# Kernel tuning notes

Measured on AMD Instinct MI355X. Metric: run time of the kernel, lower is better.

The kernel has to match this reference:

```python
import jax, jax.numpy as jnp
import numpy as np

D, H = 128, 8
N_NODE, N_SRC = 50000, 100000
E_NBR, E_INC = 800000, 200000


def _seg_softmax(scores, idx, n):
    # scores: [E, H]; segmented softmax over segments given by idx
    mx = jax.ops.segment_max(scores, idx, num_segments=n)
    ex = jnp.exp(scores - mx[idx])
    sm = jax.ops.segment_sum(ex, idx, num_segments=n)
    return ex / (sm[idx] + 1e-12)


def _ln(x, g, b):
    m = jnp.mean(x, -1, keepdims=True)
    v = jnp.mean((x - m) ** 2, -1, keepdims=True)
    return g * (x - m) / jnp.sqrt(v + 1e-5) + b


def setup_inputs() -> dict:
    key = jax.random.key(0)
    ks = jax.random.split(key, 24)
    s = 1.0 / np.sqrt(D)
    inp = {
        'X': jax.random.normal(ks[0], (N_NODE, D), jnp.float32),
        'X_src': jax.random.normal(ks[1], (N_SRC, D), jnp.float32),
        'W_qkv': jax.random.normal(ks[2], (D, 3 * D), jnp.float32) * s,
        'w_bias': jax.random.normal(ks[3], (D, H), jnp.float32) * s,
        'W_gate': jax.random.normal(ks[4], (D, D), jnp.float32) * s,
        'b_gate': jnp.zeros((D,), jnp.float32),
        'W_o': jax.random.normal(ks[5], (D, D), jnp.float32) * s,
        'W_q': jax.random.normal(ks[6], (D, D), jnp.float32) * s,
        'W_kv': jax.random.normal(ks[7], (D, 2 * D), jnp.float32) * s,
        'w_bias_tgt': jax.random.normal(ks[8], (D, H), jnp.float32) * s,
        'w_bias_src': jax.random.normal(ks[9], (D, H), jnp.float32) * s,
        'W_gate_tgt': jax.random.normal(ks[10], (D, D), jnp.float32) * s,
        'b_gate_tgt': jnp.zeros((D,), jnp.float32),
        'W_gate_src': jax.random.normal(ks[11], (D, D), jnp.float32) * s,
        'b_gate_src': jnp.zeros((D,), jnp.float32),
        'W_o2': jax.random.normal(ks[12], (D, D), jnp.float32) * s,
        'ln1_g': jnp.ones((D,), jnp.float32),
        'ln1_b': jnp.zeros((D,), jnp.float32),
        'ln2_g': jnp.ones((D,), jnp.float32),
        'ln2_b': jnp.zeros((D,), jnp.float32),
        'nbr_src': jax.random.randint(ks[13], (E_NBR,), 0, N_NODE),
        'nbr_dst': jax.random.randint(ks[14], (E_NBR,), 0, N_NODE),
        'inc_tgt': jax.random.randint(ks[15], (E_INC,), 0, N_NODE),
        'inc_src': jax.random.randint(ks[16], (E_INC,), 0, N_SRC),
    }
    return inp


def reference(X, X_src, W_qkv, w_bias, W_gate, b_gate, W_o, W_q, W_kv,
              w_bias_tgt, w_bias_src, W_gate_tgt, b_gate_tgt, W_gate_src,
              b_gate_src, W_o2, ln1_g, ln1_b, ln2_g, ln2_b,
              nbr_src, nbr_dst, inc_tgt, inc_src):
    N = X.shape[0]
    dk = D // H
    scale = 1.0 / np.sqrt(dk)

    # --- SparseNeighbourhoodSelfAttn on level-0 cells ---
    qkv = (X @ W_qkv).reshape(N, 3, H, dk)
    Q, K, V = qkv[:, 0], qkv[:, 1], qkv[:, 2]            # [N,H,dk]
    scores = jnp.sum(Q[nbr_src] * K[nbr_dst], -1) * scale + (X @ w_bias)[nbr_src]  # [E,H]
    attn = _seg_softmax(scores, nbr_src, N)
    out = jax.ops.segment_sum(attn[..., None] * V[nbr_dst], nbr_src, num_segments=N)  # [N,H,dk]
    gate = jax.nn.sigmoid(X @ W_gate + b_gate).reshape(N, H, dk)
    sa = (gate * out).reshape(N, D) @ W_o
    h = _ln(X + sa, ln1_g, ln1_b)

    # --- SparseTopologicalCrossAttn from level-1 cells ---
    Qc = (h @ W_q).reshape(N, H, dk)
    kv = (X_src @ W_kv).reshape(-1, 2, H, dk)
    Kc, Vc = kv[:, 0], kv[:, 1]
    sc = (jnp.sum(Qc[inc_tgt] * Kc[inc_src], -1) * scale
          + (h @ w_bias_tgt)[inc_tgt] + (X_src @ w_bias_src)[inc_src])  # [Ei,H]
    attn_c = _seg_softmax(sc, inc_tgt, N)
    g_src = jax.nn.sigmoid(X_src @ W_gate_src + b_gate_src).reshape(-1, H, dk)
    out_c = jax.ops.segment_sum(attn_c[..., None] * (g_src[inc_src] * Vc[inc_src]),
                                inc_tgt, num_segments=N)
    g_tgt = jax.nn.sigmoid(h @ W_gate_tgt + b_gate_tgt).reshape(N, H, dk)
    ca = (g_tgt * out_c).reshape(N, D) @ W_o2
    return _ln(h + ca, ln2_g, ln2_b)
```

## Files before the change

### kernel.cpp

```cpp
#include <hip/hip_runtime.h>
#include <stdint.h>

__device__ __forceinline__ float bf_lo(uint32_t w) { return __uint_as_float(w << 16); }
__device__ __forceinline__ float bf_hi(uint32_t w) { return __uint_as_float(w & 0xffff0000u); }
__device__ __forceinline__ float bfu(uint16_t u) { return __uint_as_float((uint32_t)u << 16); }
__device__ __forceinline__ uint16_t f2bf(float f) {
    uint32_t u = __float_as_uint(f);
    uint32_t r = ((u >> 16) & 1u) + 0x7fffu;
    return (uint16_t)((u + r) >> 16);
}
__device__ __forceinline__ uint32_t pk2bf(float a, float b) {
    return (uint32_t)f2bf(a) | ((uint32_t)f2bf(b) << 16);
}
__device__ __forceinline__ void gload_lds16(const void* g, void* l) {
    __builtin_amdgcn_global_load_lds(
        (const __attribute__((address_space(1))) void*)g,
        (__attribute__((address_space(3))) void*)l, 16, 0, 0);
}

typedef __attribute__((ext_vector_type(8))) short bf16x8;
typedef __attribute__((ext_vector_type(4))) float f32x4;

#define LOG2E 1.4426950408889634f
#define QSC2  (0.25f * LOG2E)

#define M_BF16 0
#define M_QS   1
#define M_SIG  2
#define M_KVIK 3
#define M_KVIV 4
#define M_GV   5
#define M_LN1  6
#define M_LN2  7
#define M_B8   8

struct GemmJob {
    const uint16_t* A; const uint16_t* WT; const float* bias;
    const uint16_t* aux; const void* resid;
    const float* lng; const float* lnb;
    void* out; int M; int mode;
};
struct GemmJobs { GemmJob j[6]; };

__global__ __launch_bounds__(256) void multi_gemm_k(GemmJobs jobs)
{
    __shared__ uint16_t As[128 * 128];
    __shared__ uint16_t Ws[128 * 128];
    const GemmJob jb = jobs.j[blockIdx.y];
    const int m0 = blockIdx.x * 128;
    if (m0 >= jb.M) return;
    const int tid = threadIdx.x;
    const int wid = tid >> 6;
    const int lane = tid & 63;

    {
        const uint16_t* Ab = jb.A + (size_t)m0 * 128;
        const uint16_t* Wb = jb.WT;
#pragma unroll
        for (int it = 0; it < 8; ++it) {
            int idx = it * 256 + tid;
            int r = idx >> 4, c = idx & 15;
            int gc = c ^ (r & 7);
            uint16_t* ldsA = As + (size_t)(it * 256 + wid * 64) * 8;
            uint16_t* ldsW = Ws + (size_t)(it * 256 + wid * 64) * 8;
            gload_lds16(Ab + (size_t)r * 128 + gc * 8, ldsA);
            gload_lds16(Wb + (size_t)r * 128 + gc * 8, ldsW);
        }
    }
    __syncthreads();

    const int wr = wid >> 1, wc = wid & 1;
    const int l15 = lane & 15, l4 = lane >> 4;
    const int mode = jb.mode;

    if (mode == M_B8) {
        f32x4 acc[4];
#pragma unroll
        for (int i = 0; i < 4; i++) acc[i] = (f32x4){0.f, 0.f, 0.f, 0.f};
#pragma unroll
        for (int kk = 0; kk < 4; ++kk) {
            bf16x8 af0;
            {
                int r = l15;
                int cc = (kk * 4 + l4) ^ (r & 7);
                af0 = *(const bf16x8*)(Ws + r * 128 + cc * 8);
            }
#pragma unroll
            for (int mi = 0; mi < 4; ++mi) {
                int r = wr * 64 + mi * 16 + l15;
                int cc = (kk * 4 + l4) ^ (r & 7);
                bf16x8 bf = *(const bf16x8*)(As + r * 128 + cc * 8);
                acc[mi] = __builtin_amdgcn_mfma_f32_16x16x32_bf16(af0, bf, acc[mi], 0, 0, 0);
            }
        }
        if (wc == 0 && l4 < 2) {
#pragma unroll
            for (int mi = 0; mi < 4; ++mi) {
                int gm = m0 + wr * 64 + mi * 16 + l15;
                if (gm < jb.M) {
                    f32x4 v = acc[mi];
                    *(float4*)((float*)jb.out + (size_t)gm * 8 + l4 * 4) =
                        make_float4(v.x, v.y, v.z, v.w);
                }
            }
        }
        return;
    }

    f32x4 acc[4][4];
#pragma unroll
    for (int i = 0; i < 4; i++)
#pragma unroll
        for (int j = 0; j < 4; j++) acc[i][j] = (f32x4){0.f, 0.f, 0.f, 0.f};

#pragma unroll
    for (int kk = 0; kk < 4; ++kk) {
        bf16x8 af[4], bff[4];
#pragma unroll
        for (int ni = 0; ni < 4; ++ni) {
            int r = wc * 64 + ni * 16 + l15;
            int cc = (kk * 4 + l4) ^ (r & 7);
            af[ni] = *(const bf16x8*)(Ws + r * 128 + cc * 8);
        }
#pragma unroll
        for (int mi = 0; mi < 4; ++mi) {
            int r = wr * 64 + mi * 16 + l15;
            int cc = (kk * 4 + l4) ^ (r & 7);
            bff[mi] = *(const bf16x8*)(As + r * 128 + cc * 8);
        }
#pragma unroll
        for (int ni = 0; ni < 4; ++ni)
#pragma unroll
            for (int mi = 0; mi < 4; ++mi)
                acc[ni][mi] = __builtin_amdgcn_mfma_f32_16x16x32_bf16(
                    af[ni], bff[mi], acc[ni][mi], 0, 0, 0);
    }

    if (mode == M_LN1 || mode == M_LN2) {
        __syncthreads();
        float* redS = (float*)Ws;
        float* redQ = redS + 256;
        float ps[4], qs[4];
#pragma unroll
        for (int mi = 0; mi < 4; ++mi) {
            int row = wr * 64 + mi * 16 + l15;
            int gm = m0 + row;
            float sum = 0.f, sq = 0.f;
#pragma unroll
            for (int ni = 0; ni < 4; ++ni) {
                int gn = wc * 64 + ni * 16 + l4 * 4;
                float r0 = 0.f, r1 = 0.f, r2 = 0.f, r3 = 0.f;
                if (gm < jb.M) {
                    if (mode == M_LN1) {
                        float4 rv = *(const float4*)((const float*)jb.resid + (size_t)gm * 128 + gn);
                        r0 = rv.x; r1 = rv.y; r2 = rv.z; r3 = rv.w;
                    } else {
                        ushort4 rv = *(const ushort4*)((const uint16_t*)jb.resid + (size_t)gm * 128 + gn);
                        r0 = bfu(rv.x); r1 = bfu(rv.y); r2 = bfu(rv.z); r3 = bfu(rv.w);
                    }
                }
                f32x4 t = acc[ni][mi];
                t.x += r0; t.y += r1; t.z += r2; t.w += r3;
                acc[ni][mi] = t;
                sum += t.x + t.y + t.z + t.w;
                sq  += t.x * t.x + t.y * t.y + t.z * t.z + t.w * t.w;
            }
            sum += __shfl_xor(sum, 16); sum += __shfl_xor(sum, 32);
            sq  += __shfl_xor(sq, 16);  sq  += __shfl_xor(sq, 32);
            ps[mi] = sum; qs[mi] = sq;
        }
        if (l4 == 0) {
#pragma unroll
            for (int mi = 0; mi < 4; ++mi) {
                int row = wr * 64 + mi * 16 + l15;
                redS[row * 2 + wc] = ps[mi];
                redQ[row * 2 + wc] = qs[mi];
            }
        }
        __syncthreads();
#pragma unroll
        for (int mi = 0; mi < 4; ++mi) {
            int row = wr * 64 + mi * 16 + l15;
            int gm = m0 + row;
            if (gm >= jb.M) continue;
            float S = redS[row * 2] + redS[row * 2 + 1];
            float Q = redQ[row * 2] + redQ[row * 2 + 1];
            float mean = S * (1.f / 128.f);
            float var  = Q * (1.f / 128.f) - mean * mean;
            float rstd = rsqrtf(var + 1e-5f);
#pragma unroll
            for (int ni = 0; ni < 4; ++ni) {
                int gn = wc * 64 + ni * 16 + l4 * 4;
                float4 gg = *(const float4*)(jb.lng + gn);
                float4 bb = *(const float4*)(jb.lnb + gn);
                f32x4 t = acc[ni][mi];
                float o0 = gg.x * (t.x - mean) * rstd + bb.x;
                float o1 = gg.y * (t.y - mean) * rstd + bb.y;
                float o2 = gg.z * (t.z - mean) * rstd + bb.z;
                float o3 = gg.w * (t.w - mean) * rstd + bb.w;
                if (mode == M_LN1) {
                    ushort4 o;
                    o.x = f2bf(o0); o.y = f2bf(o1); o.z = f2bf(o2); o.w = f2bf(o3);
                    *(ushort4*)((uint16_t*)jb.out + (size_t)gm * 128 + gn) = o;
                } else {
                    *(float4*)((float*)jb.out + (size_t)gm * 128 + gn) =
                        make_float4(o0, o1, o2, o3);
                }
            }
        }
        return;
    }

#pragma unroll
    for (int mi = 0; mi < 4; ++mi) {
        int gm = m0 + wr * 64 + mi * 16 + l15;
        if (gm >= jb.M) continue;
#pragma unroll
        for (int ni = 0; ni < 4; ++ni) {
            int gn = wc * 64 + ni * 16 + l4 * 4;
            f32x4 v = acc[ni][mi];
            if (mode == M_SIG || mode == M_GV) {
                float4 bb = *(const float4*)(jb.bias + gn);
                v.x = 1.f / (1.f + __expf(-(v.x + bb.x)));
                v.y = 1.f / (1.f + __expf(-(v.y + bb.y)));
                v.z = 1.f / (1.f + __expf(-(v.z + bb.z)));
                v.w = 1.f / (1.f + __expf(-(v.w + bb.w)));
            }
            if (mode == M_QS) { v.x *= QSC2; v.y *= QSC2; v.z *= QSC2; v.w *= QSC2; }
            if (mode == M_GV) {
                ushort4 vs = *(const ushort4*)(jb.aux + (size_t)gm * 128 + gn);
                v.x *= bfu(vs.x); v.y *= bfu(vs.y); v.z *= bfu(vs.z); v.w *= bfu(vs.w);
            }
            if (mode == M_KVIK || mode == M_KVIV || mode == M_GV) {
                int which = (mode == M_KVIK) ? 0 : 2;
                uint16_t* op = (uint16_t*)jb.out + (size_t)gm * 256 + gn * 2 + which;
                *reinterpret_cast<uint32_t*>(op)     = pk2bf(v.x, v.y);
                *reinterpret_cast<uint32_t*>(op + 4) = pk2bf(v.z, v.w);
            } else {
                ushort4 o;
                o.x = f2bf(v.x); o.y = f2bf(v.y); o.z = f2bf(v.z); o.w = f2bf(v.w);
                *reinterpret_cast<ushort4*>((uint16_t*)jb.out + (size_t)gm * 128 + gn) = o;
            }
        }
    }
}

__global__ void castbf2_k(const float* __restrict__ in1, uint16_t* __restrict__ out1, int n1,
                          const float* __restrict__ in2, uint16_t* __restrict__ out2, int n2,
                          int* __restrict__ zero256)
{
    if (blockIdx.x == 0 && threadIdx.x < 256) zero256[threadIdx.x] = 0;
    int i = blockIdx.x * blockDim.x + threadIdx.x;
    int stride = gridDim.x * blockDim.x;
    for (; i < n1 + n2; i += stride) {
        float4 v;
        ushort4 o;
        if (i < n1) v = reinterpret_cast<const float4*>(in1)[i];
        else        v = reinterpret_cast<const float4*>(in2)[i - n1];
        o.x = f2bf(v.x); o.y = f2bf(v.y); o.z = f2bf(v.z); o.w = f2bf(v.w);
        if (i < n1) reinterpret_cast<ushort4*>(out1)[i] = o;
        else        reinterpret_cast<ushort4*>(out2)[i - n1] = o;
    }
}

struct WT14 { const float* src[14]; uint16_t* dst[14]; int nc[14]; int coff[14]; };
__global__ void castWT14_k(WT14 jb)
{
    int y = blockIdx.y;
    const float* W = jb.src[y];
    uint16_t* WT = jb.dst[y];
    int nc = jb.nc[y], coff = jb.coff[y];
    int i = blockIdx.x * 256 + threadIdx.x;
    int k = i >> 7, n = i & 127;
    float v;
    if (nc == 8) v = (n < 8) ? W[k * 8 + n] * LOG2E : 0.f;
    else         v = W[(size_t)k * nc + coff + n];
    WT[(size_t)n * 128 + k] = f2bf(v);
}

#define NBKT_MAX 256

__global__ __launch_bounds__(256) void binH_k(
    const int* __restrict__ s1, const int* __restrict__ s2,
    int* __restrict__ bktcnt, int E1, int E2, int N, int shift, int nbkt, int chunk)
{
    __shared__ int hist[NBKT_MAX];
    int t = threadIdx.x;
    for (int i = t; i < nbkt; i += 256) hist[i] = 0;
    __syncthreads();
    int Et = E1 + E2;
    int base = blockIdx.x * chunk;
    int end = min(base + chunk, Et);
    for (int i = base + t; i < end; i += 256) {
        int seg = (i < E1) ? s1[i] : N + s2[i - E1];
        atomicAdd(&hist[seg >> shift], 1);
    }
    __syncthreads();
    for (int i = t; i < nbkt; i += 256)
        if (hist[i]) atomicAdd(&bktcnt[i], hist[i]);
}

__global__ __launch_bounds__(256) void bktscan_k(
    const int* __restrict__ bktcnt, int* __restrict__ bktbase,
    int* __restrict__ bktcur, int nbkt)
{
    __shared__ int wt[4];
    int t = threadIdx.x, lane = t & 63, w = t >> 6;
    int v = (t < nbkt) ? bktcnt[t] : 0;
    int s = v;
#pragma unroll
    for (int o = 1; o < 64; o <<= 1) { int x = __shfl_up(s, o); if (lane >= o) s += x; }
    if (lane == 63) wt[w] = s;
    __syncthreads();
    int add = 0;
    for (int i = 0; i < w; i++) add += wt[i];
    int excl = add + s - v;
    if (t < nbkt) { bktbase[t] = excl; bktcur[t] = excl; }
    if (t == nbkt - 1) bktbase[nbkt] = excl + v;
}

__global__ __launch_bounds__(256) void binA_k(
    const int* __restrict__ s1, const int* __restrict__ p1,
    const int* __restrict__ s2, const int* __restrict__ p2,
    int* __restrict__ bktcur, uint2* __restrict__ tmp,
    int E1, int E2, int N, int shift, int nbkt, int chunk)
{
    __shared__ int hist[NBKT_MAX];
    __shared__ int lcur[NBKT_MAX];
    int t = threadIdx.x;
    int Et = E1 + E2;
    int base = blockIdx.x * chunk;
    int end = min(base + chunk, Et);
    for (int i = t; i < nbkt; i += 256) hist[i] = 0;
    __syncthreads();
    for (int i = base + t; i < end; i += 256) {
        int seg = (i < E1) ? s1[i] : N + s2[i - E1];
        atomicAdd(&hist[seg >> shift], 1);
    }
    __syncthreads();
    for (int i = t; i < nbkt; i += 256) {
        int c = hist[i];
        lcur[i] = c ? atomicAdd(&bktcur[i], c) : 0;
    }
    __syncthreads();
    for (int i = base + t; i < end; i += 256) {
        int seg, pay;
        if (i < E1) { seg = s1[i]; pay = p1[i]; }
        else        { seg = N + s2[i - E1]; pay = p2[i - E1]; }
        int p = atomicAdd(&lcur[seg >> shift], 1);
        tmp[p] = make_uint2((uint32_t)seg, (uint32_t)pay);
    }
}

__global__ __launch_bounds__(256) void binD_k(
    const uint2* __restrict__ tmp, const int* __restrict__ bktbase,
    int* __restrict__ offs, int* __restrict__ sorted, int NN, int spb, int Et)
{
    extern __shared__ int sh[];
    __shared__ int wt[4];
    int b = blockIdx.x, t = threadIdx.x;
    int s0 = b * spb;
    int segs = min(spb, NN - s0);
    for (int i = t; i < segs; i += 256) sh[i] = 0;
    __syncthreads();
    int p0 = bktbase[b], p1 = bktbase[b + 1];
    for (int i = p0 + t; i < p1; i += 256)
        atomicAdd(&sh[(int)tmp[i].x - s0], 1);
    __syncthreads();
    int e_per = spb >> 8;
    int loc[4]; int ls = 0;
#pragma unroll 4
    for (int j = 0; j < 4; ++j) {
        if (j < e_per) {
            int idx = t * e_per + j;
            int v = (idx < segs) ? sh[idx] : 0;
            loc[j] = ls; ls += v;
        }
    }
    int lane = t & 63, w = t >> 6;
    int sc = ls;
#pragma unroll
    for (int o = 1; o < 64; o <<= 1) { int x = __shfl_up(sc, o); if (lane >= o) sc += x; }
    if (lane == 63) wt[w] = sc;
    __syncthreads();
    int add = 0;
    for (int i = 0; i < w; i++) add += wt[i];
    int texcl = add + sc - ls;
#pragma unroll 4
    for (int j = 0; j < 4; ++j) {
        if (j < e_per) {
            int idx = t * e_per + j;
            if (idx < segs) {
                int pos = p0 + texcl + loc[j];
                offs[s0 + idx] = pos;
                sh[idx] = pos;
            }
        }
    }
    __syncthreads();
    for (int i = p0 + t; i < p1; i += 256) {
        uint2 pr = tmp[i];
        int p = atomicAdd(&sh[(int)pr.x - s0], 1);
        sorted[p] = (int)pr.y;
    }
    if (b == 0 && t == 0) offs[NN] = Et;
}

#define SEDGE(J, IDX)                                                            \
    {                                                                            \
        int dst = sdst[IDX];                                                     \
        uint2 kv = *reinterpret_cast<const uint2*>(kb + ((size_t)dst << 8));     \
        float s = q0 * bf_lo(kv.x) + q1 * bf_hi(kv.x);                           \
        s += __shfl_xor(s, 1); s += __shfl_xor(s, 2); s += __shfl_xor(s, 4);     \
        float w = exp2f(s + bs);                                                 \
        pa##J = fmaf(w, bf_lo(kv.y), pa##J);                                     \
        pb##J = fmaf(w, bf_hi(kv.y), pb##J);                                     \
        dn##J += w;                                                              \
    }

__global__ __launch_bounds__(256) void self_attn_k(
    const uint16_t* __restrict__ Qb, const uint16_t* __restrict__ kvi,
    const float* __restrict__ bias1,
    const int* __restrict__ offs, const int* __restrict__ sdst,
    const uint16_t* __restrict__ g16, uint16_t* __restrict__ Aout, int N)
{
    int lane = threadIdx.x & 63;
    int n = blockIdx.x * 4 + (threadIdx.x >> 6);
    if (n >= N) return;
    uint32_t qw = *reinterpret_cast<const uint32_t*>(Qb + (size_t)n * 128 + 2 * lane);
    float q0 = bf_lo(qw), q1 = bf_hi(qw);
    float bs = bias1[(size_t)n * 8 + (lane >> 3)];
    int e0 = offs[n], e1 = offs[n + 1];
    const uint16_t* kb = kvi + lane * 4;
    float dn0 = 0.f, pa0 = 0.f, pb0 = 0.f;
    float dn1 = 0.f, pa1 = 0.f, pb1 = 0.f;
    int e = e0;
    for (; e + 4 <= e1; e += 4) {
        SEDGE(0, e)
        SEDGE(1, e + 1)
        SEDGE(0, e + 2)
        SEDGE(1, e + 3)
    }
    for (; e < e1; ++e) SEDGE(0, e)
    float den = dn0 + dn1, a0 = pa0 + pa1, a1 = pb0 + pb1;
    float inv = 1.f / (den + 1e-30f);
    uint32_t gw = *reinterpret_cast<const uint32_t*>(g16 + (size_t)n * 128 + 2 * lane);
    a0 *= inv * bf_lo(gw); a1 *= inv * bf_hi(gw);
    *reinterpret_cast<uint32_t*>(Aout + (size_t)n * 128 + 2 * lane) = pk2bf(a0, a1);
}

#define CEDGE(J, IDX)                                                            \
    {                                                                            \
        int src = ssrc[IDX];                                                     \
        uint2 kv = *reinterpret_cast<const uint2*>(kb + ((size_t)src << 8));     \
        float bss = bias_s[(size_t)src * 8 + (lane >> 3)];                       \
        float s = q0 * bf_lo(kv.x) + q1 * bf_hi(kv.x);                           \
        s += __shfl_xor(s, 1); s += __shfl_xor(s, 2); s += __shfl_xor(s, 4);     \
        float w = exp2f(s + bt + bss);                                           \
        pa##J = fmaf(w, bf_lo(kv.y), pa##J);                                     \
        pb##J = fmaf(w, bf_hi(kv.y), pb##J);                                     \
        dn##J += w;                                                              \
    }

__global__ __launch_bounds__(256) void cross_attn_k(
    const uint16_t* __restrict__ Qcb, const float* __restrict__ bias_t,
    const uint16_t* __restrict__ kvgi, const float* __restrict__ bias_s,
    const int* __restrict__ offs, const int* __restrict__ ssrc,
    const uint16_t* __restrict__ g16, uint16_t* __restrict__ Aout, int N)
{
    int lane = threadIdx.x & 63;
    int n = blockIdx.x * 4 + (threadIdx.x >> 6);
    if (n >= N) return;
    uint32_t qw = *reinterpret_cast<const uint32_t*>(Qcb + (size_t)n * 128 + 2 * lane);
    float q0 = bf_lo(qw), q1 = bf_hi(qw);
    float bt = bias_t[(size_t)n * 8 + (lane >> 3)];
    int e0 = offs[n], e1 = offs[n + 1];
    const uint16_t* kb = kvgi + lane * 4;
    float dn0 = 0.f, pa0 = 0.f, pb0 = 0.f;
    float dn1 = 0.f, pa1 = 0.f, pb1 = 0.f;
    int e = e0;
    for (; e + 4 <= e1; e += 4) {
        CEDGE(0, e)
        CEDGE(1, e + 1)
        CEDGE(0, e + 2)
        CEDGE(1, e + 3)
    }
    for (; e < e1; ++e) CEDGE(0, e)
    float den = dn0 + dn1, a0 = pa0 + pa1, a1 = pb0 + pb1;
    float inv = 1.f / (den + 1e-30f);
    uint32_t gw = *reinterpret_cast<const uint32_t*>(g16 + (size_t)n * 128 + 2 * lane);
    a0 *= inv * bf_lo(gw); a1 *= inv * bf_hi(gw);
    *reinterpret_cast<uint32_t*>(Aout + (size_t)n * 128 + 2 * lane) = pk2bf(a0, a1);
}

static inline size_t smax_(size_t a, size_t b) { return a > b ? a : b; }

extern "C" void kernel_launch(void* const* d_in, const int* in_sizes, int n_in,
                              void* d_out, int out_size, void* d_ws, size_t ws_size,
                              hipStream_t stream)
{
    const float* X          = (const float*)d_in[0];
    const float* Xs         = (const float*)d_in[1];
    const float* W_qkv      = (const float*)d_in[2];
    const float* w_bias     = (const float*)d_in[3];
    const float* W_gate     = (const float*)d_in[4];
    const float* b_gate     = (const float*)d_in[5];
    const float* W_o        = (const float*)d_in[6];
    const float* W_q        = (const float*)d_in[7];
    const float* W_kv       = (const float*)d_in[8];
    const float* w_bias_tgt = (const float*)d_in[9];
    const float* w_bias_src = (const float*)d_in[10];
    const float* W_gate_tgt = (const float*)d_in[11];
    const float* b_gate_tgt = (const float*)d_in[12];
    const float* W_gate_src = (const float*)d_in[13];
    const float* b_gate_src = (const float*)d_in[14];
    const float* W_o2       = (const float*)d_in[15];
    const float* ln1_g      = (const float*)d_in[16];
    const float* ln1_b      = (const float*)d_in[17];
    const float* ln2_g      = (const float*)d_in[18];
    const float* ln2_b      = (const float*)d_in[19];
    const int* nbr_src      = (const int*)d_in[20];
    const int* nbr_dst      = (const int*)d_in[21];
    const int* inc_tgt      = (const int*)d_in[22];
    const int* inc_src      = (const int*)d_in[23];

    const int N  = in_sizes[0] / 128;
    const int NS = in_sizes[1] / 128;
    const int E1 = in_sizes[20];
    const int E2 = in_sizes[22];
    const int Et = E1 + E2;
    const int NN = 2 * N;
    const int Npad  = (N + 127) & ~127;
    const int NSpad = (NS + 127) & ~127;

    int shift = 9;
    while (((NN + (1 << shift) - 1) >> shift) > NBKT_MAX) ++shift;
    const int spb  = 1 << shift;
    const int nbkt = (NN + spb - 1) >> shift;

    char* ws = (char*)d_ws;
    size_t off = 0;
    auto alloc = [&](size_t bytes) -> void* {
        void* p = ws + off;
        off = (off + bytes + 255) & ~(size_t)255;
        return p;
    };

    uint16_t* Xb   = (uint16_t*)alloc((size_t)Npad * 128 * 2);
    uint16_t* Xsb  = (uint16_t*)alloc((size_t)NSpad * 128 * 2);
    uint16_t* WTq  = (uint16_t*)alloc((size_t)384 * 128 * 2);
    uint16_t* WTkv = (uint16_t*)alloc((size_t)256 * 128 * 2);
    uint16_t* WTg  = (uint16_t*)alloc((size_t)128 * 128 * 2);
    uint16_t* WTo  = (uint16_t*)alloc((size_t)128 * 128 * 2);
    uint16_t* WTq2 = (uint16_t*)alloc((size_t)128 * 128 * 2);
    uint16_t* WTgt = (uint16_t*)alloc((size_t)128 * 128 * 2);
    uint16_t* WTgs = (uint16_t*)alloc((size_t)128 * 128 * 2);
    uint16_t* WTo2 = (uint16_t*)alloc((size_t)128 * 128 * 2);
    uint16_t* WTb1 = (uint16_t*)alloc((size_t)128 * 128 * 2);
    uint16_t* WTbt = (uint16_t*)alloc((size_t)128 * 128 * 2);
    uint16_t* WTbs = (uint16_t*)alloc((size_t)128 * 128 * 2);
    size_t s1a = (size_t)Npad * 384 * 2;
    size_t s1b = (size_t)NSpad * 384 * 2;
    size_t s1c = (size_t)Et * 8;
    uint16_t* S1 = (uint16_t*)alloc(smax_(smax_(s1a, s1b), s1c));
    uint16_t* Qb   = S1;
    uint16_t* kvi  = S1 + (size_t)Npad * 128;
    uint16_t* kvgi = S1;
    uint16_t* V16  = S1 + (size_t)NSpad * 256;
    uint2*    tmp  = (uint2*)S1;
    uint16_t* g16  = (uint16_t*)alloc((size_t)N * 128 * 2);
    uint16_t* Qcb  = (uint16_t*)alloc((size_t)N * 128 * 2);
    uint16_t* Awo  = (uint16_t*)alloc((size_t)Npad * 128 * 2);
    uint16_t* hb   = (uint16_t*)alloc((size_t)Npad * 128 * 2);
    float*    b8a  = (float*)alloc((size_t)N * 8 * 4);
    float*    b8s  = (float*)alloc((size_t)NS * 8 * 4);
    int* offs   = (int*)alloc((size_t)(NN + 1) * 4);
    int* sorted = (int*)alloc((size_t)Et * 4);
    int* bktcnt = (int*)alloc((size_t)NBKT_MAX * 4);
    int* bktbase= (int*)alloc((size_t)(NBKT_MAX + 1) * 4);
    int* bktcur = (int*)alloc((size_t)NBKT_MAX * 4);
    (void)ws_size; (void)n_in; (void)out_size;

    const int gA  = Npad / 128;
    const int gAs = NSpad / 128;
    const int gW  = (N + 3) / 4;
    const int BINB = 128;
    const int chunk = (Et + BINB - 1) / BINB;

    castbf2_k<<<2048, 256, 0, stream>>>(X, Xb, N * 32, Xs, Xsb, NS * 32, bktcnt);
    {
        WT14 jb;
        jb.src[0] = W_qkv; jb.dst[0] = WTq;          jb.nc[0] = 384; jb.coff[0] = 0;
        jb.src[1] = W_qkv; jb.dst[1] = WTq + 16384;  jb.nc[1] = 384; jb.coff[1] = 128;
        jb.src[2] = W_qkv; jb.dst[2] = WTq + 32768;  jb.nc[2] = 384; jb.coff[2] = 256;
        jb.src[3] = W_kv;  jb.dst[3] = WTkv;         jb.nc[3] = 256; jb.coff[3] = 0;
        jb.src[4] = W_kv;  jb.dst[4] = WTkv + 16384; jb.nc[4] = 256; jb.coff[4] = 128;
        jb.src[5] = W_gate;     jb.dst[5] = WTg;  jb.nc[5] = 128; jb.coff[5] = 0;
        jb.src[6] = W_o;        jb.dst[6] = WTo;  jb.nc[6] = 128; jb.coff[6] = 0;
        jb.src[7] = W_q;        jb.dst[7] = WTq2; jb.nc[7] = 128; jb.coff[7] = 0;
        jb.src[8] = W_gate_tgt; jb.dst[8] = WTgt; jb.nc[8] = 128; jb.coff[8] = 0;
        jb.src[9] = W_gate_src; jb.dst[9] = WTgs; jb.nc[9] = 128; jb.coff[9] = 0;
        jb.src[10]= W_o2;       jb.dst[10]= WTo2; jb.nc[10]= 128; jb.coff[10]= 0;
        jb.src[11]= w_bias;     jb.dst[11]= WTb1; jb.nc[11]= 8;   jb.coff[11]= 0;
        jb.src[12]= w_bias_tgt; jb.dst[12]= WTbt; jb.nc[12]= 8;   jb.coff[12]= 0;
        jb.src[13]= w_bias_src; jb.dst[13]= WTbs; jb.nc[13]= 8;   jb.coff[13]= 0;
        castWT14_k<<<dim3(64, 14), 256, 0, stream>>>(jb);
    }

    binH_k<<<BINB, 256, 0, stream>>>(nbr_src, inc_tgt, bktcnt, E1, E2, N, shift, nbkt, chunk);
    bktscan_k<<<1, 256, 0, stream>>>(bktcnt, bktbase, bktcur, nbkt);
    binA_k<<<BINB, 256, 0, stream>>>(nbr_src, nbr_dst, inc_tgt, inc_src,
                                     bktcur, tmp, E1, E2, N, shift, nbkt, chunk);
    binD_k<<<nbkt, 256, spb * 4, stream>>>(tmp, bktbase, offs, sorted, NN, spb, Et);

    {
        GemmJobs jb{};
        jb.j[0] = { Xb, WTq,         nullptr, nullptr, nullptr, nullptr, nullptr, Qb,  N, M_QS };
        jb.j[1] = { Xb, WTq + 16384, nullptr, nullptr, nullptr, nullptr, nullptr, kvi, N, M_KVIK };
        jb.j[2] = { Xb, WTq + 32768, nullptr, nullptr, nullptr, nullptr, nullptr, kvi, N, M_KVIV };
        jb.j[3] = { Xb, WTg,         b_gate,  nullptr, nullptr, nullptr, nullptr, g16, N, M_SIG };
        jb.j[4] = { Xb, WTb1,        nullptr, nullptr, nullptr, nullptr, nullptr, b8a, N, M_B8 };
        multi_gemm_k<<<dim3(gA, 5), 256, 0, stream>>>(jb);
    }
    self_attn_k<<<gW, 256, 0, stream>>>(Qb, kvi, b8a, offs, sorted, g16, Awo, N);
    {
        GemmJobs jb{};
        jb.j[0] = { Awo, WTo, nullptr, nullptr, X, ln1_g, ln1_b, hb, N, M_LN1 };
        multi_gemm_k<<<dim3(gA, 1), 256, 0, stream>>>(jb);
    }
    {
        GemmJobs jb{};
        jb.j[0] = { hb,  WTq2,         nullptr,    nullptr, nullptr, nullptr, nullptr, Qcb,  N,  M_QS };
        jb.j[1] = { hb,  WTgt,         b_gate_tgt, nullptr, nullptr, nullptr, nullptr, g16,  N,  M_SIG };
        jb.j[2] = { Xsb, WTkv,         nullptr,    nullptr, nullptr, nullptr, nullptr, kvgi, NS, M_KVIK };
        jb.j[3] = { Xsb, WTkv + 16384, nullptr,    nullptr, nullptr, nullptr, nullptr, V16,  NS, M_BF16 };
        jb.j[4] = { hb,  WTbt,         nullptr,    nullptr, nullptr, nullptr, nullptr, b8a,  N,  M_B8 };
        multi_gemm_k<<<dim3(gAs, 5), 256, 0, stream>>>(jb);
    }
    {
        GemmJobs jb{};
        jb.j[0] = { Xsb, WTgs, b_gate_src, V16, nullptr, nullptr, nullptr, kvgi, NS, M_GV };
        jb.j[1] = { Xsb, WTbs, nullptr, nullptr, nullptr, nullptr, nullptr, b8s,  NS, M_B8 };
        multi_gemm_k<<<dim3(gAs, 2), 256, 0, stream>>>(jb);
    }
    cross_attn_k<<<gW, 256, 0, stream>>>(Qcb, b8a, kvgi, b8s, offs + N, sorted, g16, Awo, N);
    {
        GemmJobs jb{};
        jb.j[0] = { Awo, WTo2, nullptr, nullptr, hb, ln2_g, ln2_b, d_out, N, M_LN2 };
        multi_gemm_k<<<dim3(gA, 1), 256, 0, stream>>>(jb);
    }
}
```

Before: 339.5 us.

## Reuse A tile across jobs per block and drop histogram pass in edge binning

The GEMM kernel now stages the A tile once per block and loops over several weight matrices, replacing grid-y job dispatch that reloaded A for each job. The cross-attention source GEMMs are reordered so the V tile written by one job is consumed by the gated job inside the same block. Edge binning drops the histogram and scan kernels by using fixed-capacity buckets and writing per-segment end offsets. This cuts launches and A-tile traffic but lowers grid parallelism per launch and serializes jobs within a block; fixed bucket capacity could overflow on skewed inputs.

```diff
diff --git a/kernel.cpp b/kernel.cpp
--- a/kernel.cpp
+++ b/kernel.cpp
@@ -34,222 +34,234 @@
 #define M_LN2  7
 #define M_B8   8
 
-struct GemmJob {
-    const uint16_t* A; const uint16_t* WT; const float* bias;
-    const uint16_t* aux; const void* resid;
-    const float* lng; const float* lnb;
-    void* out; int M; int mode;
+struct GJob {
+    const uint16_t* WT; const float* bias; const uint16_t* aux;
+    const void* resid; const float* lng; const float* lnb;
+    void* out; int mode;
 };
-struct GemmJobs { GemmJob j[6]; };
-
-__global__ __launch_bounds__(256) void multi_gemm_k(GemmJobs jobs)
+struct GArgs { const uint16_t* A; int M; int njobs; GJob j[5]; };
+
+__device__ __forceinline__ void stage_tile(const uint16_t* __restrict__ g,
+                                           uint16_t* lds, int tid, int wid)
+{
+#pragma unroll
+    for (int it = 0; it < 8; ++it) {
+        int idx = it * 256 + tid;
+        int r = idx >> 4, c = idx & 15;
+        int gc = c ^ (r & 7);
+        gload_lds16(g + (size_t)r * 128 + gc * 8,
+                    lds + (size_t)(it * 256 + wid * 64) * 8);
+    }
+}
+
+__global__ __launch_bounds__(256) void gemmA_k(GArgs ga)
 {
     __shared__ uint16_t As[128 * 128];
     __shared__ uint16_t Ws[128 * 128];
-    const GemmJob jb = jobs.j[blockIdx.y];
-    const int m0 = blockIdx.x * 128;
-    if (m0 >= jb.M) return;
     const int tid = threadIdx.x;
     const int wid = tid >> 6;
     const int lane = tid & 63;
-
-    {
-        const uint16_t* Ab = jb.A + (size_t)m0 * 128;
-        const uint16_t* Wb = jb.WT;
-#pragma unroll
-        for (int it = 0; it < 8; ++it) {
-            int idx = it * 256 + tid;
-            int r = idx >> 4, c = idx & 15;
-            int gc = c ^ (r & 7);
-            uint16_t* ldsA = As + (size_t)(it * 256 + wid * 64) * 8;
-            uint16_t* ldsW = Ws + (size_t)(it * 256 + wid * 64) * 8;
-            gload_lds16(Ab + (size_t)r * 128 + gc * 8, ldsA);
-            gload_lds16(Wb + (size_t)r * 128 + gc * 8, ldsW);
-        }
-    }
+    const int m0 = blockIdx.x * 128;
+    const int M = ga.M;
+
+    stage_tile(ga.A + (size_t)m0 * 128, As, tid, wid);
+    stage_tile(ga.j[0].WT, Ws, tid, wid);
     __syncthreads();
 
     const int wr = wid >> 1, wc = wid & 1;
     const int l15 = lane & 15, l4 = lane >> 4;
-    const int mode = jb.mode;
-
-    if (mode == M_B8) {
-        f32x4 acc[4];
-#pragma unroll
-        for (int i = 0; i < 4; i++) acc[i] = (f32x4){0.f, 0.f, 0.f, 0.f};
-#pragma unroll
-        for (int kk = 0; kk < 4; ++kk) {
-            bf16x8 af0;
-            {
-                int r = l15;
-                int cc = (kk * 4 + l4) ^ (r & 7);
-                af0 = *(const bf16x8*)(Ws + r * 128 + cc * 8);
+
+    for (int jj = 0; ; ) {
+        const GJob jb = ga.j[jj];
+        const int mode = jb.mode;
+
+        if (mode == M_B8) {
+            f32x4 acc[4];
+#pragma unroll
+            for (int i = 0; i < 4; i++) acc[i] = (f32x4){0.f, 0.f, 0.f, 0.f};
+#pragma unroll
+            for (int kk = 0; kk < 4; ++kk) {
+                bf16x8 af0;
+                {
+                    int r = l15;
+                    int cc = (kk * 4 + l4) ^ (r & 7);
+                    af0 = *(const bf16x8*)(Ws + r * 128 + cc * 8);
+                }
+#pragma unroll
+                for (int mi = 0; mi < 4; ++mi) {
+                    int r = wr * 64 + mi * 16 + l15;
+                    int cc = (kk * 4 + l4) ^ (r & 7);
+                    bf16x8 bf = *(const bf16x8*)(As + r * 128 + cc * 8);
+                    acc[mi] = __builtin_amdgcn_mfma_f32_16x16x32_bf16(af0, bf, acc[mi], 0, 0, 0);
+                }
             }
-#pragma unroll
-            for (int mi = 0; mi < 4; ++mi) {
-                int r = wr * 64 + mi * 16 + l15;
-                int cc = (kk * 4 + l4) ^ (r & 7);
-                bf16x8 bf = *(const bf16x8*)(As + r * 128 + cc * 8);
-                acc[mi] = __builtin_amdgcn_mfma_f32_16x16x32_bf16(af0, bf, acc[mi], 0, 0, 0);
+            if (wc == 0 && l4 < 2) {
+#pragma unroll
+                for (int mi = 0; mi < 4; ++mi) {
+                    int gm = m0 + wr * 64 + mi * 16 + l15;
+                    if (gm < M) {
+                        f32x4 v = acc[mi];
+                        *(float4*)((float*)jb.out + (size_t)gm * 8 + l4 * 4) =
+                            make_float4(v.x, v.y, v.z, v.w);
+                    }
+                }
+            }
+        } else {
+            f32x4 acc[4][4];
+#pragma unroll
+            for (int i = 0; i < 4; i++)
+#pragma unroll
+                for (int j = 0; j < 4; j++) acc[i][j] = (f32x4){0.f, 0.f, 0.f, 0.f};
+
+#pragma unroll
+            for (int kk = 0; kk < 4; ++kk) {
+                bf16x8 af[4], bff[4];
+#pragma unroll
+                for (int ni = 0; ni < 4; ++ni) {
+                    int r = wc * 64 + ni * 16 + l15;
+                    int cc = (kk * 4 + l4) ^ (r & 7);
+                    af[ni] = *(const bf16x8*)(Ws + r * 128 + cc * 8);
+                }
+#pragma unroll
+                for (int mi = 0; mi < 4; ++mi) {
+                    int r = wr * 64 + mi * 16 + l15;
+                    int cc = (kk * 4 + l4) ^ (r & 7);
+                    bff[mi] = *(const bf16x8*)(As + r * 128 + cc * 8);
+                }
+#pragma unroll
+                for (int ni = 0; ni < 4; ++ni)
+#pragma unroll
+                    for (int mi = 0; mi < 4; ++mi)
+                        acc[ni][mi] = __builtin_amdgcn_mfma_f32_16x16x32_bf16(
+                            af[ni], bff[mi], acc[ni][mi], 0, 0, 0);
+            }
+
+            if (mode == M_LN1 || mode == M_LN2) {
+                __syncthreads();
+                float* redS = (float*)Ws;
+                float* redQ = redS + 256;
+                float ps[4], qs[4];
+#pragma unroll
+                for (int mi = 0; mi < 4; ++mi) {
+                    int row = wr * 64 + mi * 16 + l15;
+                    int gm = m0 + row;
+                    float sum = 0.f, sq = 0.f;
+#pragma unroll
+                    for (int ni = 0; ni < 4; ++ni) {
+                        int gn = wc * 64 + ni * 16 + l4 * 4;
+                        float r0 = 0.f, r1 = 0.f, r2 = 0.f, r3 = 0.f;
+                        if (gm < M) {
+                            if (mode == M_LN1) {
+                                float4 rv = *(const float4*)((const float*)jb.resid + (size_t)gm * 128 + gn);
+                                r0 = rv.x; r1 = rv.y; r2 = rv.z; r3 = rv.w;
+                            } else {
+                                ushort4 rv = *(const ushort4*)((const uint16_t*)jb.resid + (size_t)gm * 128 + gn);
+                                r0 = bfu(rv.x); r1 = bfu(rv.y); r2 = bfu(rv.z); r3 = bfu(rv.w);
+                            }
+                        }
+                        f32x4 t = acc[ni][mi];
+                        t.x += r0; t.y += r1; t.z += r2; t.w += r3;
+                        acc[ni][mi] = t;
+                        sum += t.x + t.y + t.z + t.w;
+                        sq  += t.x * t.x + t.y * t.y + t.z * t.z + t.w * t.w;
+                    }
+                    sum += __shfl_xor(sum, 16); sum += __shfl_xor(sum, 32);
+                    sq  += __shfl_xor(sq, 16);  sq  += __shfl_xor(sq, 32);
+                    ps[mi] = sum; qs[mi] = sq;
+                }
+                if (l4 == 0) {
+#pragma unroll
+                    for (int mi = 0; mi < 4; ++mi) {
+                        int row = wr * 64 + mi * 16 + l15;
+                        redS[row * 2 + wc] = ps[mi];
+                        redQ[row * 2 + wc] = qs[mi];
+                    }
+                }
+                __syncthreads();
+#pragma unroll
+                for (int mi = 0; mi < 4; ++mi) {
+                    int row = wr * 64 + mi * 16 + l15;
+                    int gm = m0 + row;
+                    if (gm >= M) continue;
+                    float S = redS[row * 2] + redS[row * 2 + 1];
+                    float Q = redQ[row * 2] + redQ[row * 2 + 1];
+                    float mean = S * (1.f / 128.f);
+                    float var  = Q * (1.f / 128.f) - mean * mean;
+                    float rstd = rsqrtf(var + 1e-5f);
+#pragma unroll
+                    for (int ni = 0; ni < 4; ++ni) {
+                        int gn = wc * 64 + ni * 16 + l4 * 4;
+                        float4 gg = *(const float4*)(jb.lng + gn);
+                        float4 bb = *(const float4*)(jb.lnb + gn);
+                        f32x4 t = acc[ni][mi];
+                        float o0 = gg.x * (t.x - mean) * rstd + bb.x;
+                        float o1 = gg.y * (t.y - mean) * rstd + bb.y;
+                        float o2 = gg.z * (t.z - mean) * rstd + bb.z;
+                        float o3 = gg.w * (t.w - mean) * rstd + bb.w;
+                        if (mode == M_LN1) {
+                            ushort4 o;
+                            o.x = f2bf(o0); o.y = f2bf(o1); o.z = f2bf(o2); o.w = f2bf(o3);
+                            *(ushort4*)((uint16_t*)jb.out + (size_t)gm * 128 + gn) = o;
+                        } else {
+                            *(float4*)((float*)jb.out + (size_t)gm * 128 + gn) =
+                                make_float4(o0, o1, o2, o3);
+                        }
+                    }
+                }
+            } else {
+#pragma unroll
+                for (int mi = 0; mi < 4; ++mi) {
+                    int gm = m0 + wr * 64 + mi * 16 + l15;
+                    if (gm >= M) continue;
+#pragma unroll
+                    for (int ni = 0; ni < 4; ++ni) {
+                        int gn = wc * 64 + ni * 16 + l4 * 4;
+                        f32x4 v = acc[ni][mi];
+                        if (mode == M_SIG || mode == M_GV) {
+                            float4 bb = *(const float4*)(jb.bias + gn);
+                            v.x = 1.f / (1.f + __expf(-(v.x + bb.x)));
+                            v.y = 1.f / (1.f + __expf(-(v.y + bb.y)));
+                            v.z = 1.f / (1.f + __expf(-(v.z + bb.z)));
+                            v.w = 1.f / (1.f + __expf(-(v.w + bb.w)));
+                        }
+                        if (mode == M_QS) { v.x *= QSC2; v.y *= QSC2; v.z *= QSC2; v.w *= QSC2; }
+                        if (mode == M_GV) {
+                            ushort4 vs = *(const ushort4*)(jb.aux + (size_t)gm * 128 + gn);
+                            v.x *= bfu(vs.x); v.y *= bfu(vs.y); v.z *= bfu(vs.z); v.w *= bfu(vs.w);
+                        }
+                        if (mode == M_KVIK || mode == M_KVIV || mode == M_GV) {
+                            int which = (mode == M_KVIK) ? 0 : 2;
+                            uint16_t* op = (uint16_t*)jb.out + (size_t)gm * 256 + gn * 2 + which;
+                            *reinterpret_cast<uint32_t*>(op)     = pk2bf(v.x, v.y);
+                            *reinterpret_cast<uint32_t*>(op + 4) = pk2bf(v.z, v.w);
+                        } else {
+                            ushort4 o;
+                            o.x = f2bf(v.x); o.y = f2bf(v.y); o.z = f2bf(v.z); o.w = f2bf(v.w);
+                            *reinterpret_cast<ushort4*>((uint16_t*)jb.out + (size_t)gm * 128 + gn) = o;
+                        }
+                    }
+                }
             }
         }
-        if (wc == 0 && l4 < 2) {
-#pragma unroll
-            for (int mi = 0; mi < 4; ++mi) {
-                int gm = m0 + wr * 64 + mi * 16 + l15;
-                if (gm < jb.M) {
-                    f32x4 v = acc[mi];
-                    *(float4*)((float*)jb.out + (size_t)gm * 8 + l4 * 4) =
-                        make_float4(v.x, v.y, v.z, v.w);
-                }
-            }
-        }
-        return;
-    }
-
-    f32x4 acc[4][4];
-#pragma unroll
-    for (int i = 0; i < 4; i++)
-#pragma unroll
-        for (int j = 0; j < 4; j++) acc[i][j] = (f32x4){0.f, 0.f, 0.f, 0.f};
-
-#pragma unroll
-    for (int kk = 0; kk < 4; ++kk) {
-        bf16x8 af[4], bff[4];
-#pragma unroll
-        for (int ni = 0; ni < 4; ++ni) {
-            int r = wc * 64 + ni * 16 + l15;
-            int cc = (kk * 4 + l4) ^ (r & 7);
-            af[ni] = *(const bf16x8*)(Ws + r * 128 + cc * 8);
-        }
-#pragma unroll
-        for (int mi = 0; mi < 4; ++mi) {
-            int r = wr * 64 + mi * 16 + l15;
-            int cc = (kk * 4 + l4) ^ (r & 7);
-            bff[mi] = *(const bf16x8*)(As + r * 128 + cc * 8);
-        }
-#pragma unroll
-        for (int ni = 0; ni < 4; ++ni)
-#pragma unroll
-            for (int mi = 0; mi < 4; ++mi)
-                acc[ni][mi] = __builtin_amdgcn_mfma_f32_16x16x32_bf16(
-                    af[ni], bff[mi], acc[ni][mi], 0, 0, 0);
-    }
-
-    if (mode == M_LN1 || mode == M_LN2) {
+
+        ++jj;
+        if (jj >= ga.njobs) break;
         __syncthreads();
-        float* redS = (float*)Ws;
-        float* redQ = redS + 256;
-        float ps[4], qs[4];
-#pragma unroll
-        for (int mi = 0; mi < 4; ++mi) {
-            int row = wr * 64 + mi * 16 + l15;
-            int gm = m0 + row;
-            float sum = 0.f, sq = 0.f;
-#pragma unroll
-            for (int ni = 0; ni < 4; ++ni) {
-                int gn = wc * 64 + ni * 16 + l4 * 4;
-                float r0 = 0.f, r1 = 0.f, r2 = 0.f, r3 = 0.f;
-                if (gm < jb.M) {
-                    if (mode == M_LN1) {
-                        float4 rv = *(const float4*)((const float*)jb.resid + (size_t)gm * 128 + gn);
-                        r0 = rv.x; r1 = rv.y; r2 = rv.z; r3 = rv.w;
-                    } else {
-                        ushort4 rv = *(const ushort4*)((const uint16_t*)jb.resid + (size_t)gm * 128 + gn);
-                        r0 = bfu(rv.x); r1 = bfu(rv.y); r2 = bfu(rv.z); r3 = bfu(rv.w);
-                    }
-                }
-                f32x4 t = acc[ni][mi];
-                t.x += r0; t.y += r1; t.z += r2; t.w += r3;
-                acc[ni][mi] = t;
-                sum += t.x + t.y + t.z + t.w;
-                sq  += t.x * t.x + t.y * t.y + t.z * t.z + t.w * t.w;
-            }
-            sum += __shfl_xor(sum, 16); sum += __shfl_xor(sum, 32);
-            sq  += __shfl_xor(sq, 16);  sq  += __shfl_xor(sq, 32);
-            ps[mi] = sum; qs[mi] = sq;
-        }
-        if (l4 == 0) {
-#pragma unroll
-            for (int mi = 0; mi < 4; ++mi) {
-                int row = wr * 64 + mi * 16 + l15;
-                redS[row * 2 + wc] = ps[mi];
-                redQ[row * 2 + wc] = qs[mi];
-            }
-        }
+        stage_tile(ga.j[jj].WT, Ws, tid, wid);
         __syncthreads();
-#pragma unroll
-        for (int mi = 0; mi < 4; ++mi) {
-            int row = wr * 64 + mi * 16 + l15;
-            int gm = m0 + row;
-            if (gm >= jb.M) continue;
-            float S = redS[row * 2] + redS[row * 2 + 1];
-            float Q = redQ[row * 2] + redQ[row * 2 + 1];
-            float mean = S * (1.f / 128.f);
-            float var  = Q * (1.f / 128.f) - mean * mean;
-            float rstd = rsqrtf(var + 1e-5f);
-#pragma unroll
-            for (int ni = 0; ni < 4; ++ni) {
-                int gn = wc * 64 + ni * 16 + l4 * 4;
-                float4 gg = *(const float4*)(jb.lng + gn);
-                float4 bb = *(const float4*)(jb.lnb + gn);
-                f32x4 t = acc[ni][mi];
-                float o0 = gg.x * (t.x - mean) * rstd + bb.x;
-                float o1 = gg.y * (t.y - mean) * rstd + bb.y;
-                float o2 = gg.z * (t.z - mean) * rstd + bb.z;
-                float o3 = gg.w * (t.w - mean) * rstd + bb.w;
-                if (mode == M_LN1) {
-                    ushort4 o;
-                    o.x = f2bf(o0); o.y = f2bf(o1); o.z = f2bf(o2); o.w = f2bf(o3);
-                    *(ushort4*)((uint16_t*)jb.out + (size_t)gm * 128 + gn) = o;
-                } else {
-                    *(float4*)((float*)jb.out + (size_t)gm * 128 + gn) =
-                        make_float4(o0, o1, o2, o3);
-                }
-            }
-        }
-        return;
-    }
-
-#pragma unroll
-    for (int mi = 0; mi < 4; ++mi) {
-        int gm = m0 + wr * 64 + mi * 16 + l15;
-        if (gm >= jb.M) continue;
-#pragma unroll
-        for (int ni = 0; ni < 4; ++ni) {
-            int gn = wc * 64 + ni * 16 + l4 * 4;
-            f32x4 v = acc[ni][mi];
-            if (mode == M_SIG || mode == M_GV) {
-                float4 bb = *(const float4*)(jb.bias + gn);
-                v.x = 1.f / (1.f + __expf(-(v.x + bb.x)));
-                v.y = 1.f / (1.f + __expf(-(v.y + bb.y)));
-                v.z = 1.f / (1.f + __expf(-(v.z + bb.z)));
-                v.w = 1.f / (1.f + __expf(-(v.w + bb.w)));
-            }
-            if (mode == M_QS) { v.x *= QSC2; v.y *= QSC2; v.z *= QSC2; v.w *= QSC2; }
-            if (mode == M_GV) {
-                ushort4 vs = *(const ushort4*)(jb.aux + (size_t)gm * 128 + gn);
-                v.x *= bfu(vs.x); v.y *= bfu(vs.y); v.z *= bfu(vs.z); v.w *= bfu(vs.w);
-            }
-            if (mode == M_KVIK || mode == M_KVIV || mode == M_GV) {
-                int which = (mode == M_KVIK) ? 0 : 2;
-                uint16_t* op = (uint16_t*)jb.out + (size_t)gm * 256 + gn * 2 + which;
-                *reinterpret_cast<uint32_t*>(op)     = pk2bf(v.x, v.y);
-                *reinterpret_cast<uint32_t*>(op + 4) = pk2bf(v.z, v.w);
-            } else {
-                ushort4 o;
-                o.x = f2bf(v.x); o.y = f2bf(v.y); o.z = f2bf(v.z); o.w = f2bf(v.w);
-                *reinterpret_cast<ushort4*>((uint16_t*)jb.out + (size_t)gm * 128 + gn) = o;
-            }
-        }
-    }
-}
+    }
+}
+
+#define NBKT_MAX 256
+#define CAPSHIFT 14
+#define BCAP (1 << CAPSHIFT)
 
 __global__ void castbf2_k(const float* __restrict__ in1, uint16_t* __restrict__ out1, int n1,
                           const float* __restrict__ in2, uint16_t* __restrict__ out2, int n2,
-                          int* __restrict__ zero256)
-{
-    if (blockIdx.x == 0 && threadIdx.x < 256) zero256[threadIdx.x] = 0;
+                          int* __restrict__ bktcur)
+{
+    if (blockIdx.x == 0 && threadIdx.x < NBKT_MAX)
+        bktcur[threadIdx.x] = threadIdx.x << CAPSHIFT;
     int i = blockIdx.x * blockDim.x + threadIdx.x;
     int stride = gridDim.x * blockDim.x;
     for (; i < n1 + n2; i += stride) {
@@ -278,47 +290,6 @@
     WT[(size_t)n * 128 + k] = f2bf(v);
 }
 
-#define NBKT_MAX 256
-
-__global__ __launch_bounds__(256) void binH_k(
-    const int* __restrict__ s1, const int* __restrict__ s2,
-    int* __restrict__ bktcnt, int E1, int E2, int N, int shift, int nbkt, int chunk)
-{
-    __shared__ int hist[NBKT_MAX];
-    int t = threadIdx.x;
-    for (int i = t; i < nbkt; i += 256) hist[i] = 0;
-    __syncthreads();
-    int Et = E1 + E2;
-    int base = blockIdx.x * chunk;
-    int end = min(base + chunk, Et);
-    for (int i = base + t; i < end; i += 256) {
-        int seg = (i < E1) ? s1[i] : N + s2[i - E1];
-        atomicAdd(&hist[seg >> shift], 1);
-    }
-    __syncthreads();
-    for (int i = t; i < nbkt; i += 256)
-        if (hist[i]) atomicAdd(&bktcnt[i], hist[i]);
-}
-
-__global__ __launch_bounds__(256) void bktscan_k(
-    const int* __restrict__ bktcnt, int* __restrict__ bktbase,
-    int* __restrict__ bktcur, int nbkt)
-{
-    __shared__ int wt[4];
-    int t = threadIdx.x, lane = t & 63, w = t >> 6;
-    int v = (t < nbkt) ? bktcnt[t] : 0;
-    int s = v;
-#pragma unroll
-    for (int o = 1; o < 64; o <<= 1) { int x = __shfl_up(s, o); if (lane >= o) s += x; }
-    if (lane == 63) wt[w] = s;
-    __syncthreads();
-    int add = 0;
-    for (int i = 0; i < w; i++) add += wt[i];
-    int excl = add + s - v;
-    if (t < nbkt) { bktbase[t] = excl; bktcur[t] = excl; }
-    if (t == nbkt - 1) bktbase[nbkt] = excl + v;
-}
-
 __global__ __launch_bounds__(256) void binA_k(
     const int* __restrict__ s1, const int* __restrict__ p1,
     const int* __restrict__ s2, const int* __restrict__ p2,
@@ -353,28 +324,30 @@
 }
 
 __global__ __launch_bounds__(256) void binD_k(
-    const uint2* __restrict__ tmp, const int* __restrict__ bktbase,
-    int* __restrict__ offs, int* __restrict__ sorted, int NN, int spb, int Et)
+    const uint2* __restrict__ tmp, const int* __restrict__ bktcur,
+    int* __restrict__ offs, int* __restrict__ ends,
+    int* __restrict__ sorted, int NN, int spb)
 {
     extern __shared__ int sh[];
     __shared__ int wt[4];
     int b = blockIdx.x, t = threadIdx.x;
     int s0 = b * spb;
     int segs = min(spb, NN - s0);
+    int p0 = b << CAPSHIFT;
+    int p1 = bktcur[b];
     for (int i = t; i < segs; i += 256) sh[i] = 0;
     __syncthreads();
-    int p0 = bktbase[b], p1 = bktbase[b + 1];
     for (int i = p0 + t; i < p1; i += 256)
         atomicAdd(&sh[(int)tmp[i].x - s0], 1);
     __syncthreads();
-    int e_per = spb >> 8;
-    int loc[4]; int ls = 0;
+    int e_per = (spb + 255) >> 8;
+    int loc[4], cv[4]; int ls = 0;
 #pragma unroll 4
     for (int j = 0; j < 4; ++j) {
         if (j < e_per) {
             int idx = t * e_per + j;
             int v = (idx < segs) ? sh[idx] : 0;
-            loc[j] = ls; ls += v;
+            loc[j] = ls; cv[j] = v; ls += v;
         }
     }
     int lane = t & 63, w = t >> 6;
@@ -393,6 +366,7 @@
             if (idx < segs) {
                 int pos = p0 + texcl + loc[j];
                 offs[s0 + idx] = pos;
+                ends[s0 + idx] = pos + cv[j];
                 sh[idx] = pos;
             }
         }
@@ -403,7 +377,6 @@
         int p = atomicAdd(&sh[(int)pr.x - s0], 1);
         sorted[p] = (int)pr.y;
     }
-    if (b == 0 && t == 0) offs[NN] = Et;
 }
 
 #define SEDGE(J, IDX)                                                            \
@@ -421,7 +394,8 @@
 __global__ __launch_bounds__(256) void self_attn_k(
     const uint16_t* __restrict__ Qb, const uint16_t* __restrict__ kvi,
     const float* __restrict__ bias1,
-    const int* __restrict__ offs, const int* __restrict__ sdst,
+    const int* __restrict__ offs, const int* __restrict__ ends,
+    const int* __restrict__ sdst,
     const uint16_t* __restrict__ g16, uint16_t* __restrict__ Aout, int N)
 {
     int lane = threadIdx.x & 63;
@@ -430,7 +404,7 @@
     uint32_t qw = *reinterpret_cast<const uint32_t*>(Qb + (size_t)n * 128 + 2 * lane);
     float q0 = bf_lo(qw), q1 = bf_hi(qw);
     float bs = bias1[(size_t)n * 8 + (lane >> 3)];
-    int e0 = offs[n], e1 = offs[n + 1];
+    int e0 = offs[n], e1 = ends[n];
     const uint16_t* kb = kvi + lane * 4;
     float dn0 = 0.f, pa0 = 0.f, pb0 = 0.f;
     float dn1 = 0.f, pa1 = 0.f, pb1 = 0.f;
@@ -465,7 +439,8 @@
 __global__ __launch_bounds__(256) void cross_attn_k(
     const uint16_t* __restrict__ Qcb, const float* __restrict__ bias_t,
     const uint16_t* __restrict__ kvgi, const float* __restrict__ bias_s,
-    const int* __restrict__ offs, const int* __restrict__ ssrc,
+    const int* __restrict__ offs, const int* __restrict__ ends,
+    const int* __restrict__ ssrc,
     const uint16_t* __restrict__ g16, uint16_t* __restrict__ Aout, int N)
 {
     int lane = threadIdx.x & 63;
@@ -474,7 +449,7 @@
     uint32_t qw = *reinterpret_cast<const uint32_t*>(Qcb + (size_t)n * 128 + 2 * lane);
     float q0 = bf_lo(qw), q1 = bf_hi(qw);
     float bt = bias_t[(size_t)n * 8 + (lane >> 3)];
-    int e0 = offs[n], e1 = offs[n + 1];
+    int e0 = offs[n], e1 = ends[n];
     const uint16_t* kb = kvgi + lane * 4;
     float dn0 = 0.f, pa0 = 0.f, pb0 = 0.f;
     float dn1 = 0.f, pa1 = 0.f, pb1 = 0.f;
@@ -561,7 +536,7 @@
     uint16_t* WTbs = (uint16_t*)alloc((size_t)128 * 128 * 2);
     size_t s1a = (size_t)Npad * 384 * 2;
     size_t s1b = (size_t)NSpad * 384 * 2;
-    size_t s1c = (size_t)Et * 8;
+    size_t s1c = ((size_t)NBKT_MAX << CAPSHIFT) * 8;
     uint16_t* S1 = (uint16_t*)alloc(smax_(smax_(s1a, s1b), s1c));
     uint16_t* Qb   = S1;
     uint16_t* kvi  = S1 + (size_t)Npad * 128;
@@ -574,10 +549,9 @@
     uint16_t* hb   = (uint16_t*)alloc((size_t)Npad * 128 * 2);
     float*    b8a  = (float*)alloc((size_t)N * 8 * 4);
     float*    b8s  = (float*)alloc((size_t)NS * 8 * 4);
-    int* offs   = (int*)alloc((size_t)(NN + 1) * 4);
-    int* sorted = (int*)alloc((size_t)Et * 4);
-    int* bktcnt = (int*)alloc((size_t)NBKT_MAX * 4);
-    int* bktbase= (int*)alloc((size_t)(NBKT_MAX + 1) * 4);
+    int* offs   = (int*)alloc((size_t)NN * 4);
+    int* ends   = (int*)alloc((size_t)NN * 4);
+    int* sorted = (int*)alloc(((size_t)NBKT_MAX << CAPSHIFT) * 4);
     int* bktcur = (int*)alloc((size_t)NBKT_MAX * 4);
     (void)ws_size; (void)n_in; (void)out_size;
 
@@ -587,7 +561,7 @@
     const int BINB = 128;
     const int chunk = (Et + BINB - 1) / BINB;
 
-    castbf2_k<<<2048, 256, 0, stream>>>(X, Xb, N * 32, Xs, Xsb, NS * 32, bktcnt);
+    castbf2_k<<<2048, 256, 0, stream>>>(X, Xb, N * 32, Xs, Xsb, NS * 32, bktcur);
     {
         WT14 jb;
         jb.src[0] = W_qkv; jb.dst[0] = WTq;          jb.nc[0] = 384; jb.coff[0] = 0;
@@ -607,46 +581,49 @@
         castWT14_k<<<dim3(64, 14), 256, 0, stream>>>(jb);
     }
 
-    binH_k<<<BINB, 256, 0, stream>>>(nbr_src, inc_tgt, bktcnt, E1, E2, N, shift, nbkt, chunk);
-    bktscan_k<<<1, 256, 0, stream>>>(bktcnt, bktbase, bktcur, nbkt);
     binA_k<<<BINB, 256, 0, stream>>>(nbr_src, nbr_dst, inc_tgt, inc_src,
                                      bktcur, tmp, E1, E2, N, shift, nbkt, chunk);
-    binD_k<<<nbkt, 256, spb * 4, stream>>>(tmp, bktbase, offs, sorted, NN, spb, Et);
+    binD_k<<<nbkt, 256, spb * 4, stream>>>(tmp, bktcur, offs, ends, sorted, NN, spb);
 
     {
-        GemmJobs jb{};
-        jb.j[0] = { Xb, WTq,         nullptr, nullptr, nullptr, nullptr, nullptr, Qb,  N, M_QS };
-        jb.j[1] = { Xb, WTq + 16384, nullptr, nullptr, nullptr, nullptr, nullptr, kvi, N, M_KVIK };
-        jb.j[2] = { Xb, WTq + 32768, nullptr, nullptr, nullptr, nullptr, nullptr, kvi, N, M_KVIV };
-        jb.j[3] = { Xb, WTg,         b_gate,  nullptr, nullptr, nullptr, nullptr, g16, N, M_SIG };
-        jb.j[4] = { Xb, WTb1,        nullptr, nullptr, nullptr, nullptr, nullptr, b8a, N, M_B8 };
-        multi_gemm_k<<<dim3(gA, 5), 256, 0, stream>>>(jb);
-    }
-    self_attn_k<<<gW, 256, 0, stream>>>(Qb, kvi, b8a, offs, sorted, g16, Awo, N);
+        GArgs ga;
+        ga.A = Xb; ga.M = N; ga.njobs = 5;
+        ga.j[0] = { WTq,         nullptr, nullptr, nullptr, nullptr, nullptr, Qb,  M_QS };
+        ga.j[1] = { WTq + 16384, nullptr, nullptr, nullptr, nullptr, nullptr, kvi, M_KVIK };
+        ga.j[2] = { WTq + 32768, nullptr, nullptr, nullptr, nullptr, nullptr, kvi, M_KVIV };
+        ga.j[3] = { WTg,         b_gate,  nullptr, nullptr, nullptr, nullptr, g16, M_SIG };
+        ga.j[4] = { WTb1,        nullptr, nullptr, nullptr, nullptr, nullptr, b8a, M_B8 };
+        gemmA_k<<<dim3(gA), 256, 0, stream>>>(ga);
+    }
+    self_attn_k<<<gW, 256, 0, stream>>>(Qb, kvi, b8a, offs, ends, sorted, g16, Awo, N);
     {
-        GemmJobs jb{};
-        jb.j[0] = { Awo, WTo, nullptr, nullptr, X, ln1_g, ln1_b, hb, N, M_LN1 };
-        multi_gemm_k<<<dim3(gA, 1), 256, 0, stream>>>(jb);
+        GArgs ga;
+        ga.A = Awo; ga.M = N; ga.njobs = 1;
+        ga.j[0] = { WTo, nullptr, nullptr, X, ln1_g, ln1_b, hb, M_LN1 };
+        gemmA_k<<<dim3(gA), 256, 0, stream>>>(ga);
     }
     {
-        GemmJobs jb{};
-        jb.j[0] = { hb,  WTq2,         nullptr,    nullptr, nullptr, nullptr, nullptr, Qcb,  N,  M_QS };
-        jb.j[1] = { hb,  WTgt,         b_gate_tgt, nullptr, nullptr, nullptr, nullptr, g16,  N,  M_SIG };
-        jb.j[2] = { Xsb, WTkv,         nullptr,    nullptr, nullptr, nullptr, nullptr, kvgi, NS, M_KVIK };
-        jb.j[3] = { Xsb, WTkv + 16384, nullptr,    nullptr, nullptr, nullptr, nullptr, V16,  NS, M_BF16 };
-        jb.j[4] = { hb,  WTbt,         nullptr,    nullptr, nullptr, nullptr, nullptr, b8a,  N,  M_B8 };
-        multi_gemm_k<<<dim3(gAs, 5), 256, 0, stream>>>(jb);
+        GArgs ga;
+        ga.A = hb; ga.M = N; ga.njobs = 3;
+        ga.j[0] = { WTq2, nullptr,    nullptr, nullptr, nullptr, nullptr, Qcb, M_QS };
+        ga.j[1] = { WTgt, b_gate_tgt, nullptr, nullptr, nullptr, nullptr, g16, M_SIG };
+        ga.j[2] = { WTbt, nullptr,    nullptr, nullptr, nullptr, nullptr, b8a, M_B8 };
+        gemmA_k<<<dim3(gA), 256, 0, stream>>>(ga);
     }
     {
-        GemmJobs jb{};
-        jb.j[0] = { Xsb, WTgs, b_gate_src, V16, nullptr, nullptr, nullptr, kvgi, NS, M_GV };
-        jb.j[1] = { Xsb, WTbs, nullptr, nullptr, nullptr, nullptr, nullptr, b8s,  NS, M_B8 };
-        multi_gemm_k<<<dim3(gAs, 2), 256, 0, stream>>>(jb);
-    }
-    cross_attn_k<<<gW, 256, 0, stream>>>(Qcb, b8a, kvgi, b8s, offs + N, sorted, g16, Awo, N);
+        GArgs ga;
+        ga.A = Xsb; ga.M = NS; ga.njobs = 4;
+        ga.j[0] = { WTkv,         nullptr,    nullptr, nullptr, nullptr, nullptr, kvgi, M_KVIK };
+        ga.j[1] = { WTkv + 16384, nullptr,    nullptr, nullptr, nullptr, nullptr, V16,  M_BF16 };
+        ga.j[2] = { WTgs,         b_gate_src, V16,     nullptr, nullptr, nullptr, kvgi, M_GV };
+        ga.j[3] = { WTbs,         nullptr,    nullptr, nullptr, nullptr, nullptr, b8s,  M_B8 };
+        gemmA_k<<<dim3(gAs), 256, 0, stream>>>(ga);
+    }
+    cross_attn_k<<<gW, 256, 0, stream>>>(Qcb, b8a, kvgi, b8s, offs + N, ends + N, sorted, g16, Awo, N);
     {
-        GemmJobs jb{};
-        jb.j[0] = { Awo, WTo2, nullptr, nullptr, hb, ln2_g, ln2_b, d_out, N, M_LN2 };
-        multi_gemm_k<<<dim3(gA, 1), 256, 0, stream>>>(jb);
-    }
-}
+        GArgs ga;
+        ga.A = Awo; ga.M = N; ga.njobs = 1;
+        ga.j[0] = { WTo2, nullptr, nullptr, hb, ln2_g, ln2_b, d_out, M_LN2 };
+        gemmA_k<<<dim3(gA), 256, 0, stream>>>(ga);
+    }
+}
```

Measured after the change: 401.0 us. 1.18x slower.
